# Kernel tuning notes

Hardware: AMD Instinct MI355X
Metric: run time of the kernel (lower is better)

The kernel has to match this reference:

```python
import jax, jax.numpy as jnp
import numpy as np

HEADS = 4
HEAD_DIM = 32
IN_DIM = 128
N_TRIG = 48
N_SPAN = 128


def build_edges(T, S):
    # nodes are (trig r, span c) flattened row-major: n = r*S + c
    N = T * S
    nodes = jnp.arange(N, dtype=jnp.int32)
    r = nodes // S
    c = nodes % S
    # same-row neighbors (includes self loop once): [N, S]
    row_nb = r[:, None] * S + jnp.arange(S, dtype=jnp.int32)[None, :]
    # same-column neighbors excluding own row: [N, T-1]
    t_idx = jnp.arange(T - 1, dtype=jnp.int32)[None, :]
    t = t_idx + (t_idx >= r[:, None]).astype(jnp.int32)
    col_nb = t * S + c[:, None]
    deg = S + T - 1
    src = jnp.concatenate([row_nb, col_nb], axis=1).reshape(-1)  # [N*deg]
    dst = jnp.repeat(nodes, deg)
    return src, dst, N


def gat_conv(x, src, dst, N, W, att_src, att_dst, bias):
    # PyG GATConv (eval mode, dropout off), concat=True.
    # W: [in, H*Hd]; att_src/att_dst: [H, Hd]; bias: [H*Hd]
    h = (x @ W).reshape(N, HEADS, HEAD_DIM)          # [N,H,Hd]
    a_src = jnp.sum(h * att_src[None], axis=-1)      # [N,H]
    a_dst = jnp.sum(h * att_dst[None], axis=-1)      # [N,H]
    e = jax.nn.leaky_relu(a_src[src] + a_dst[dst], negative_slope=0.2)  # [E,H]
    # scatter-softmax over incoming edges per destination node
    m = jax.ops.segment_max(e, dst, num_segments=N)  # [N,H]
    ex = jnp.exp(e - m[dst])
    denom = jax.ops.segment_sum(ex, dst, num_segments=N)
    alpha = ex / denom[dst]                          # [E,H]
    msg = alpha[:, :, None] * h[src]                 # [E,H,Hd]
    out = jax.ops.segment_sum(msg, dst, num_segments=N)  # [N,H,Hd]
    return out.reshape(N, HEADS * HEAD_DIM) + bias[None]


def setup_inputs() -> dict:
    key = jax.random.key(0)
    ks = jax.random.split(key, 9)
    D = IN_DIM
    HD = HEADS * HEAD_DIM
    inp = {
        "pair_embeddings": jax.random.normal(ks[0], (1, N_TRIG, N_SPAN, D), dtype=jnp.float32),
        "W1": jax.random.normal(ks[1], (D, HD), dtype=jnp.float32) * (2.0 / (D + HD)) ** 0.5,
        "att_src1": jax.random.normal(ks[2], (HEADS, HEAD_DIM), dtype=jnp.float32) * 0.1,
        "att_dst1": jax.random.normal(ks[3], (HEADS, HEAD_DIM), dtype=jnp.float32) * 0.1,
        "b1": jnp.zeros((HD,), dtype=jnp.float32),
        "W2": jax.random.normal(ks[4], (HD, HD), dtype=jnp.float32) * (2.0 / (HD + HD)) ** 0.5,
        "att_src2": jax.random.normal(ks[5], (HEADS, HEAD_DIM), dtype=jnp.float32) * 0.1,
        "att_dst2": jax.random.normal(ks[6], (HEADS, HEAD_DIM), dtype=jnp.float32) * 0.1,
        "b2": jnp.zeros((HD,), dtype=jnp.float32),
        "num_trigs_kept": N_TRIG,
        "num_arg_spans_kept": N_SPAN,
    }
    return inp


def reference(pair_embeddings, W1, att_src1, att_dst1, b1, W2, att_src2, att_dst2, b2, num_trigs_kept, num_arg_spans_kept):
    T, S = int(num_trigs_kept), int(num_arg_spans_kept)
    src, dst, N = build_edges(T, S)
    # batch_size == 1: slice and flatten node features
    x = pair_embeddings[0, :T, :S].reshape(N, -1)
    x = jax.nn.elu(gat_conv(x, src, dst, N, W1, att_src1, att_dst1, b1))
    x = jax.nn.elu(gat_conv(x, src, dst, N, W2, att_src2, att_dst2, b2))
    return x
```

## Files before the change

kernel.cpp:

```cpp
#include <hip/hip_runtime.h>

#define T_TRIG 48
#define S_SPAN 128
#define NN (T_TRIG * S_SPAN)
#define D 128
#define GRID 192
#define BLK 512

typedef __attribute__((ext_vector_type(8))) short sh8;
typedef __attribute__((ext_vector_type(4))) float f32x4;
typedef __attribute__((ext_vector_type(4))) unsigned short us4;

__device__ inline unsigned short f2bf(float v) {
    unsigned u = __float_as_uint(v);
    unsigned r = u + 0x7FFFu + ((u >> 16) & 1u);
    return (unsigned short)(r >> 16);
}
__device__ inline float bf2f(unsigned short b) {
    return __uint_as_float(((unsigned)b) << 16);
}

struct Params {
    const float *pe, *W1, *as1, *ad1, *b1, *W2, *as2, *ad2, *b2;
    float* out;
    unsigned int* bar;
    unsigned short *x2h, *x2l;
    float *H, *numr, *asrc, *adst, *den;
};

__device__ inline void gridbar(unsigned int* cnt) {
    asm volatile("s_waitcnt vmcnt(0)" ::: "memory");
    __syncthreads();
    if (threadIdx.x == 0) {
        asm volatile("buffer_wbl2 sc1\n\ts_waitcnt vmcnt(0)" ::: "memory");
        atomicAdd(cnt, 1u);
        while (__hip_atomic_load(cnt, __ATOMIC_RELAXED, __HIP_MEMORY_SCOPE_AGENT) < GRID)
            __builtin_amdgcn_s_sleep(8);
        asm volatile("buffer_inv sc1\n\ts_waitcnt vmcnt(0)" ::: "memory");
    }
    __syncthreads();
    __builtin_amdgcn_sched_barrier(0);
}

template<int LAYER>
__device__ void gr_phase(const Params& p, float* sm, int b, int t)
{
    const int r = b >> 2, h = b & 3;
    const int w = t >> 6, l = t & 63;
    const int c = l & 15, kg = l >> 4;
    const int row0 = r * S_SPAN + w * 16;
    const int col0 = h * 32;

    float (*sh_h)[36] = (float(*)[36])sm;
    float* sh_as = sm + 128 * 36;
    float* sh_ad = sh_as + 128;

    const float* W     = (LAYER == 1) ? p.W1  : p.W2;
    const float* att_s = (LAYER == 1) ? p.as1 : p.as2;
    const float* att_d = (LAYER == 1) ? p.ad1 : p.ad2;

    f32x4 a0 = {0,0,0,0}, a1 = {0,0,0,0};
    #pragma unroll
    for (int kc = 0; kc < 4; ++kc) {
        sh8 ah, al;
        if (LAYER == 1) {
            const float* xp = p.pe + (size_t)(row0 + c) * D + kc * 32 + kg * 8;
            float4 x0 = *(const float4*)xp;
            float4 x1 = *(const float4*)(xp + 4);
            float xs[8] = {x0.x, x0.y, x0.z, x0.w, x1.x, x1.y, x1.z, x1.w};
            #pragma unroll
            for (int i = 0; i < 8; ++i) {
                unsigned short hh = f2bf(xs[i]);
                ah[i] = (short)hh;
                al[i] = (short)f2bf(xs[i] - bf2f(hh));
            }
        } else {
            const int xi = (row0 + c) * 16 + kc * 4 + kg;
            ah = ((const sh8*)p.x2h)[xi];
            al = ((const sh8*)p.x2l)[xi];
        }
        const int kb = kc * 32 + kg * 8;
        sh8 b0h, b0l, b1h, b1l;
        #pragma unroll
        for (int i = 0; i < 8; ++i) {
            float v0 = W[(size_t)(kb + i) * D + col0 + c];
            float v1 = W[(size_t)(kb + i) * D + col0 + 16 + c];
            unsigned short h0 = f2bf(v0);
            b0h[i] = (short)h0; b0l[i] = (short)f2bf(v0 - bf2f(h0));
            unsigned short h1 = f2bf(v1);
            b1h[i] = (short)h1; b1l[i] = (short)f2bf(v1 - bf2f(h1));
        }
        a0 = __builtin_amdgcn_mfma_f32_16x16x32_bf16(ah, b0h, a0, 0, 0, 0);
        a0 = __builtin_amdgcn_mfma_f32_16x16x32_bf16(al, b0h, a0, 0, 0, 0);
        a0 = __builtin_amdgcn_mfma_f32_16x16x32_bf16(ah, b0l, a0, 0, 0, 0);
        a1 = __builtin_amdgcn_mfma_f32_16x16x32_bf16(ah, b1h, a1, 0, 0, 0);
        a1 = __builtin_amdgcn_mfma_f32_16x16x32_bf16(al, b1h, a1, 0, 0, 0);
        a1 = __builtin_amdgcn_mfma_f32_16x16x32_bf16(ah, b1l, a1, 0, 0, 0);
    }

    #pragma unroll
    for (int i = 0; i < 4; ++i) {
        const int rl = w * 16 + kg * 4 + i;
        sh_h[rl][c]      = a0[i];
        sh_h[rl][16 + c] = a1[i];
        p.H[(size_t)(row0 + kg * 4 + i) * D + col0 + c]      = a0[i];
        p.H[(size_t)(row0 + kg * 4 + i) * D + col0 + 16 + c] = a1[i];
    }

    const float as0 = att_s[col0 + c],  as1v = att_s[col0 + 16 + c];
    const float ad0 = att_d[col0 + c],  ad1v = att_d[col0 + 16 + c];
    #pragma unroll
    for (int i = 0; i < 4; ++i) {
        float ps = a0[i] * as0 + a1[i] * as1v;
        float pd = a0[i] * ad0 + a1[i] * ad1v;
        ps += __shfl_xor(ps, 1); pd += __shfl_xor(pd, 1);
        ps += __shfl_xor(ps, 2); pd += __shfl_xor(pd, 2);
        ps += __shfl_xor(ps, 4); pd += __shfl_xor(pd, 4);
        ps += __shfl_xor(ps, 8); pd += __shfl_xor(pd, 8);
        if (c == 0) {
            const int rl = w * 16 + kg * 4 + i;
            sh_as[rl] = ps;
            sh_ad[rl] = pd;
            p.asrc[(row0 + kg * 4 + i) * 4 + h] = ps;
            p.adst[(row0 + kg * 4 + i) * 4 + h] = pd;
        }
    }
    __syncthreads();

    const int d = t >> 2, fg = t & 3;
    const float ad = sh_ad[d];
    f32x4 n0 = {0,0,0,0}, n1 = {0,0,0,0};
    float dn = 0.f;
    #pragma unroll 4
    for (int cp = 0; cp < S_SPAN; ++cp) {
        float e = sh_as[cp] + ad;
        e = fmaxf(e, 0.2f * e);
        float wgt = __expf(e);
        dn += wgt;
        f32x4 h0 = *(f32x4*)&sh_h[cp][fg * 8];
        f32x4 h1 = *(f32x4*)&sh_h[cp][fg * 8 + 4];
        #pragma unroll
        for (int q = 0; q < 4; ++q) {
            n0[q] = fmaf(wgt, h0[q], n0[q]);
            n1[q] = fmaf(wgt, h1[q], n1[q]);
        }
    }
    const int node = r * S_SPAN + d;
    *(f32x4*)&p.numr[(size_t)node * D + col0 + fg * 8]     = n0;
    *(f32x4*)&p.numr[(size_t)node * D + col0 + fg * 8 + 4] = n1;
    if (fg == 0) p.den[node * 4 + h] = dn;
}

template<int LAYER>
__device__ void col_phase(const Params& p, float* sm, int b, int t)
{
    if (b >= S_SPAN) return;
    const int c = b;
    float (*sh_hc)[132] = (float(*)[132])sm;
    float (*sh_asc)[T_TRIG] = (float(*)[T_TRIG])(sm + 48 * 132);

    #pragma unroll
    for (int it = 0; it < 3; ++it) {
        int chunk = t + it * BLK;
        int tt = chunk >> 5, fc = chunk & 31;
        *(float4*)&sh_hc[tt][fc * 4] =
            *(const float4*)&p.H[(size_t)(tt * S_SPAN + c) * D + fc * 4];
    }
    if (t < 4 * T_TRIG) {
        int hh = t / T_TRIG, tt = t - hh * T_TRIG;
        sh_asc[hh][tt] = p.asrc[(tt * S_SPAN + c) * 4 + hh];
    }
    __syncthreads();

    const int f4g = t & 31, tg = t >> 5, head = f4g >> 3;
    const float* bias = (LAYER == 1) ? p.b1 : p.b2;

    f32x4 num[3] = {{0,0,0,0},{0,0,0,0},{0,0,0,0}};
    float dn[3] = {0.f, 0.f, 0.f};
    float ad[3];
    #pragma unroll
    for (int dd = 0; dd < 3; ++dd)
        ad[dd] = p.adst[((tg * 3 + dd) * S_SPAN + c) * 4 + head];

    for (int tp = 0; tp < T_TRIG; ++tp) {
        float a = sh_asc[head][tp];
        f32x4 hv = *(f32x4*)&sh_hc[tp][f4g * 4];
        #pragma unroll
        for (int dd = 0; dd < 3; ++dd) {
            float e = a + ad[dd];
            e = fmaxf(e, 0.2f * e);
            float wgt = __expf(e);
            wgt = (tp == tg * 3 + dd) ? 0.f : wgt;
            dn[dd] += wgt;
            #pragma unroll
            for (int q = 0; q < 4; ++q) num[dd][q] = fmaf(wgt, hv[q], num[dd][q]);
        }
    }

    const float4 b4 = *(const float4*)&bias[f4g * 4];
    const float bb[4] = {b4.x, b4.y, b4.z, b4.w};
    #pragma unroll
    for (int dd = 0; dd < 3; ++dd) {
        const int n = (tg * 3 + dd) * S_SPAN + c;
        f32x4 nr = *(const f32x4*)&p.numr[(size_t)n * D + f4g * 4];
        float inv = 1.f / (p.den[n * 4 + head] + dn[dd]);
        float o[4];
        #pragma unroll
        for (int q = 0; q < 4; ++q) {
            o[q] = (nr[q] + num[dd][q]) * inv + bb[q];
            o[q] = o[q] > 0.f ? o[q] : (__expf(o[q]) - 1.f);
        }
        if (LAYER == 1) {
            us4 hv4, lv4;
            #pragma unroll
            for (int q = 0; q < 4; ++q) {
                unsigned short hq = f2bf(o[q]);
                hv4[q] = hq;
                lv4[q] = f2bf(o[q] - bf2f(hq));
            }
            *(us4*)&p.x2h[(size_t)n * D + f4g * 4] = hv4;
            *(us4*)&p.x2l[(size_t)n * D + f4g * 4] = lv4;
        } else {
            float4 o4 = {o[0], o[1], o[2], o[3]};
            *(float4*)&p.out[(size_t)n * D + f4g * 4] = o4;
        }
    }
}

__global__ __launch_bounds__(BLK, 2) void fused_gat_kernel(Params p)
{
    __shared__ float sm[48 * 132 + 4 * T_TRIG];
    const int b = blockIdx.x, t = threadIdx.x;

    gr_phase<1>(p, sm, b, t);
    gridbar(p.bar + 0);
    col_phase<1>(p, sm, b, t);
    gridbar(p.bar + 32);
    gr_phase<2>(p, sm, b, t);
    gridbar(p.bar + 64);
    col_phase<2>(p, sm, b, t);
}

extern "C" void kernel_launch(void* const* d_in, const int* in_sizes, int n_in,
                              void* d_out, int out_size, void* d_ws, size_t ws_size,
                              hipStream_t stream)
{
    Params p;
    p.pe  = (const float*)d_in[0];
    p.W1  = (const float*)d_in[1];
    p.as1 = (const float*)d_in[2];
    p.ad1 = (const float*)d_in[3];
    p.b1  = (const float*)d_in[4];
    p.W2  = (const float*)d_in[5];
    p.as2 = (const float*)d_in[6];
    p.ad2 = (const float*)d_in[7];
    p.b2  = (const float*)d_in[8];
    p.out = (float*)d_out;

    char* ws = (char*)d_ws;
    size_t off = 0;
    auto alloc = [&](size_t bytes) { char* r = ws + off; off += (bytes + 255) & ~255ull; return r; };
    p.bar  = (unsigned int*)alloc(512);
    p.x2h  = (unsigned short*)alloc((size_t)NN * D * 2);
    p.x2l  = (unsigned short*)alloc((size_t)NN * D * 2);
    p.H    = (float*)alloc((size_t)NN * D * 4);
    p.numr = (float*)alloc((size_t)NN * D * 4);
    p.asrc = (float*)alloc((size_t)NN * 4 * 4);
    p.adst = (float*)alloc((size_t)NN * 4 * 4);
    p.den  = (float*)alloc((size_t)NN * 4 * 4);

    hipMemsetAsync(p.bar, 0, 512, stream);
    fused_gat_kernel<<<dim3(GRID), dim3(BLK), 0, stream>>>(p);
}
```

Measured before the change: 95.96 us.

## Double block size to 1024 threads and split work across more waves

Block size goes from 512 to 1024 threads. In the row phase each wave now computes one 16x16 output tile instead of two; attention partial sums from the two column halves are combined through shared memory with an extra barrier. In the column phase each thread handles up to two destination rows instead of three, using a non-unrolled loop with a data-dependent trip count. The aim is more parallelism per block to hide latency, at the cost of extra synchronisation, lower register budget under launch_bounds(1024,4), and an uneven row split across thread groups.

```diff
diff --git a/kernel.cpp b/kernel.cpp
--- a/kernel.cpp
+++ b/kernel.cpp
@@ -5,7 +5,7 @@
 #define NN (T_TRIG * S_SPAN)
 #define D 128
 #define GRID 192
-#define BLK 512
+#define BLK 1024
 
 typedef __attribute__((ext_vector_type(8))) short sh8;
 typedef __attribute__((ext_vector_type(4))) float f32x4;
@@ -48,18 +48,21 @@
     const int r = b >> 2, h = b & 3;
     const int w = t >> 6, l = t & 63;
     const int c = l & 15, kg = l >> 4;
-    const int row0 = r * S_SPAN + w * 16;
-    const int col0 = h * 32;
+    const int mt = w >> 1, nt = w & 1;
+    const int row0 = r * S_SPAN + mt * 16;
+    const int col0 = h * 32 + nt * 16;
 
     float (*sh_h)[36] = (float(*)[36])sm;
-    float* sh_as = sm + 128 * 36;
+    float* sh_ps = sm + 128 * 36;
+    float* sh_pd = sh_ps + 256;
+    float* sh_as = sh_pd + 256;
     float* sh_ad = sh_as + 128;
 
     const float* W     = (LAYER == 1) ? p.W1  : p.W2;
     const float* att_s = (LAYER == 1) ? p.as1 : p.as2;
     const float* att_d = (LAYER == 1) ? p.ad1 : p.ad2;
 
-    f32x4 a0 = {0,0,0,0}, a1 = {0,0,0,0};
+    f32x4 acc = {0,0,0,0};
     #pragma unroll
     for (int kc = 0; kc < 4; ++kc) {
         sh8 ah, al;
@@ -80,56 +83,56 @@
             al = ((const sh8*)p.x2l)[xi];
         }
         const int kb = kc * 32 + kg * 8;
-        sh8 b0h, b0l, b1h, b1l;
+        sh8 bh, bl;
         #pragma unroll
         for (int i = 0; i < 8; ++i) {
-            float v0 = W[(size_t)(kb + i) * D + col0 + c];
-            float v1 = W[(size_t)(kb + i) * D + col0 + 16 + c];
-            unsigned short h0 = f2bf(v0);
-            b0h[i] = (short)h0; b0l[i] = (short)f2bf(v0 - bf2f(h0));
-            unsigned short h1 = f2bf(v1);
-            b1h[i] = (short)h1; b1l[i] = (short)f2bf(v1 - bf2f(h1));
-        }
-        a0 = __builtin_amdgcn_mfma_f32_16x16x32_bf16(ah, b0h, a0, 0, 0, 0);
-        a0 = __builtin_amdgcn_mfma_f32_16x16x32_bf16(al, b0h, a0, 0, 0, 0);
-        a0 = __builtin_amdgcn_mfma_f32_16x16x32_bf16(ah, b0l, a0, 0, 0, 0);
-        a1 = __builtin_amdgcn_mfma_f32_16x16x32_bf16(ah, b1h, a1, 0, 0, 0);
-        a1 = __builtin_amdgcn_mfma_f32_16x16x32_bf16(al, b1h, a1, 0, 0, 0);
-        a1 = __builtin_amdgcn_mfma_f32_16x16x32_bf16(ah, b1l, a1, 0, 0, 0);
+            float v = W[(size_t)(kb + i) * D + col0 + c];
+            unsigned short h0 = f2bf(v);
+            bh[i] = (short)h0;
+            bl[i] = (short)f2bf(v - bf2f(h0));
+        }
+        acc = __builtin_amdgcn_mfma_f32_16x16x32_bf16(ah, bh, acc, 0, 0, 0);
+        acc = __builtin_amdgcn_mfma_f32_16x16x32_bf16(al, bh, acc, 0, 0, 0);
+        acc = __builtin_amdgcn_mfma_f32_16x16x32_bf16(ah, bl, acc, 0, 0, 0);
     }
 
     #pragma unroll
     for (int i = 0; i < 4; ++i) {
-        const int rl = w * 16 + kg * 4 + i;
-        sh_h[rl][c]      = a0[i];
-        sh_h[rl][16 + c] = a1[i];
-        p.H[(size_t)(row0 + kg * 4 + i) * D + col0 + c]      = a0[i];
-        p.H[(size_t)(row0 + kg * 4 + i) * D + col0 + 16 + c] = a1[i];
-    }
-
-    const float as0 = att_s[col0 + c],  as1v = att_s[col0 + 16 + c];
-    const float ad0 = att_d[col0 + c],  ad1v = att_d[col0 + 16 + c];
+        const int rl = mt * 16 + kg * 4 + i;
+        sh_h[rl][nt * 16 + c] = acc[i];
+        p.H[(size_t)(row0 + kg * 4 + i) * D + col0 + c] = acc[i];
+    }
+
+    const float asv = att_s[col0 + c];
+    const float adv = att_d[col0 + c];
     #pragma unroll
     for (int i = 0; i < 4; ++i) {
-        float ps = a0[i] * as0 + a1[i] * as1v;
-        float pd = a0[i] * ad0 + a1[i] * ad1v;
+        float ps = acc[i] * asv;
+        float pd = acc[i] * adv;
         ps += __shfl_xor(ps, 1); pd += __shfl_xor(pd, 1);
         ps += __shfl_xor(ps, 2); pd += __shfl_xor(pd, 2);
         ps += __shfl_xor(ps, 4); pd += __shfl_xor(pd, 4);
         ps += __shfl_xor(ps, 8); pd += __shfl_xor(pd, 8);
         if (c == 0) {
-            const int rl = w * 16 + kg * 4 + i;
-            sh_as[rl] = ps;
-            sh_ad[rl] = pd;
-            p.asrc[(row0 + kg * 4 + i) * 4 + h] = ps;
-            p.adst[(row0 + kg * 4 + i) * 4 + h] = pd;
-        }
-    }
-    __syncthreads();
-
-    const int d = t >> 2, fg = t & 3;
+            const int rl = mt * 16 + kg * 4 + i;
+            sh_ps[nt * 128 + rl] = ps;
+            sh_pd[nt * 128 + rl] = pd;
+        }
+    }
+    __syncthreads();
+    if (t < 128) {
+        float ps = sh_ps[t] + sh_ps[128 + t];
+        float pd = sh_pd[t] + sh_pd[128 + t];
+        sh_as[t] = ps;
+        sh_ad[t] = pd;
+        p.asrc[(r * S_SPAN + t) * 4 + h] = ps;
+        p.adst[(r * S_SPAN + t) * 4 + h] = pd;
+    }
+    __syncthreads();
+
+    const int d = t >> 3, fg = t & 7;
     const float ad = sh_ad[d];
-    f32x4 n0 = {0,0,0,0}, n1 = {0,0,0,0};
+    f32x4 n0 = {0,0,0,0};
     float dn = 0.f;
     #pragma unroll 4
     for (int cp = 0; cp < S_SPAN; ++cp) {
@@ -137,17 +140,12 @@
         e = fmaxf(e, 0.2f * e);
         float wgt = __expf(e);
         dn += wgt;
-        f32x4 h0 = *(f32x4*)&sh_h[cp][fg * 8];
-        f32x4 h1 = *(f32x4*)&sh_h[cp][fg * 8 + 4];
+        f32x4 hv = *(f32x4*)&sh_h[cp][fg * 4];
         #pragma unroll
-        for (int q = 0; q < 4; ++q) {
-            n0[q] = fmaf(wgt, h0[q], n0[q]);
-            n1[q] = fmaf(wgt, h1[q], n1[q]);
-        }
+        for (int q = 0; q < 4; ++q) n0[q] = fmaf(wgt, hv[q], n0[q]);
     }
     const int node = r * S_SPAN + d;
-    *(f32x4*)&p.numr[(size_t)node * D + col0 + fg * 8]     = n0;
-    *(f32x4*)&p.numr[(size_t)node * D + col0 + fg * 8 + 4] = n1;
+    *(f32x4*)&p.numr[(size_t)node * D + h * 32 + fg * 4] = n0;
     if (fg == 0) p.den[node * 4 + h] = dn;
 }
 
@@ -160,11 +158,13 @@
     float (*sh_asc)[T_TRIG] = (float(*)[T_TRIG])(sm + 48 * 132);
 
     #pragma unroll
-    for (int it = 0; it < 3; ++it) {
+    for (int it = 0; it < 2; ++it) {
         int chunk = t + it * BLK;
-        int tt = chunk >> 5, fc = chunk & 31;
-        *(float4*)&sh_hc[tt][fc * 4] =
-            *(const float4*)&p.H[(size_t)(tt * S_SPAN + c) * D + fc * 4];
+        if (chunk < 1536) {
+            int tt = chunk >> 5, fc = chunk & 31;
+            *(float4*)&sh_hc[tt][fc * 4] =
+                *(const float4*)&p.H[(size_t)(tt * S_SPAN + c) * D + fc * 4];
+        }
     }
     if (t < 4 * T_TRIG) {
         int hh = t / T_TRIG, tt = t - hh * T_TRIG;
@@ -174,23 +174,22 @@
 
     const int f4g = t & 31, tg = t >> 5, head = f4g >> 3;
     const float* bias = (LAYER == 1) ? p.b1 : p.b2;
-
-    f32x4 num[3] = {{0,0,0,0},{0,0,0,0},{0,0,0,0}};
-    float dn[3] = {0.f, 0.f, 0.f};
-    float ad[3];
-    #pragma unroll
-    for (int dd = 0; dd < 3; ++dd)
-        ad[dd] = p.adst[((tg * 3 + dd) * S_SPAN + c) * 4 + head];
+    const int nrows = (tg < 16) ? 2 : 1;
+
+    f32x4 num[2] = {{0,0,0,0},{0,0,0,0}};
+    float dn[2] = {0.f, 0.f};
+    float ad[2] = {0.f, 0.f};
+    for (int dd = 0; dd < nrows; ++dd)
+        ad[dd] = p.adst[((tg + dd * 32) * S_SPAN + c) * 4 + head];
 
     for (int tp = 0; tp < T_TRIG; ++tp) {
         float a = sh_asc[head][tp];
         f32x4 hv = *(f32x4*)&sh_hc[tp][f4g * 4];
-        #pragma unroll
-        for (int dd = 0; dd < 3; ++dd) {
+        for (int dd = 0; dd < nrows; ++dd) {
             float e = a + ad[dd];
             e = fmaxf(e, 0.2f * e);
             float wgt = __expf(e);
-            wgt = (tp == tg * 3 + dd) ? 0.f : wgt;
+            wgt = (tp == tg + dd * 32) ? 0.f : wgt;
             dn[dd] += wgt;
             #pragma unroll
             for (int q = 0; q < 4; ++q) num[dd][q] = fmaf(wgt, hv[q], num[dd][q]);
@@ -199,9 +198,8 @@
 
     const float4 b4 = *(const float4*)&bias[f4g * 4];
     const float bb[4] = {b4.x, b4.y, b4.z, b4.w};
-    #pragma unroll
-    for (int dd = 0; dd < 3; ++dd) {
-        const int n = (tg * 3 + dd) * S_SPAN + c;
+    for (int dd = 0; dd < nrows; ++dd) {
+        const int n = (tg + dd * 32) * S_SPAN + c;
         f32x4 nr = *(const f32x4*)&p.numr[(size_t)n * D + f4g * 4];
         float inv = 1.f / (p.den[n * 4 + head] + dn[dd]);
         float o[4];
@@ -227,7 +225,7 @@
     }
 }
 
-__global__ __launch_bounds__(BLK, 2) void fused_gat_kernel(Params p)
+__global__ __launch_bounds__(BLK, 4) void fused_gat_kernel(Params p)
 {
     __shared__ float sm[48 * 132 + 4 * T_TRIG];
     const int b = blockIdx.x, t = threadIdx.x;
```

New measurement: 210.4 us. 119% more time.
